# Optimization experiments

Hardware: AMD Instinct MI355X
Metric: run time of the kernel (lower is better)

## Reference

```python
import jax, jax.numpy as jnp
import numpy as np

N_NODES = 100000
N_EDGES = 1600000
D = 64

def setup_inputs() -> dict:
    key = jax.random.key(0)
    k1, k2, k3, k4 = jax.random.split(key, 4)
    feat = jax.random.normal(k1, (N_NODES, D), dtype=jnp.float32)
    src = jax.random.randint(k2, (N_EDGES,), 0, N_NODES, dtype=jnp.int32)
    dst = jax.random.randint(k3, (N_EDGES,), 0, N_NODES, dtype=jnp.int32)
    eps = jnp.zeros((1,), dtype=jnp.float32)
    W = jax.random.normal(k4, (D, D), dtype=jnp.float32) * (1.0 / np.sqrt(D))
    b = jnp.zeros((D,), dtype=jnp.float32)
    return {"feat": feat, "src": src, "dst": dst, "eps": eps, "W": W, "b": b}

def reference(feat, src, dst, eps, W, b):
    # GIN: h_i = f_Theta((1+eps)*h_i + sum_{j in N(i)} h_j)
    # Neighbor gather + segment-sum aggregation over edges (sum aggregator).
    msgs = feat[src]  # [E, D] gather of source node features
    agg = jax.ops.segment_sum(msgs, dst, num_segments=N_NODES)  # [N, D]
    rst = (1.0 + eps[0]) * feat + agg  # (1+eps)*self + aggregate
    # apply_func: Linear(D, D)
    return rst @ W + b
```

## Files before the change

### kernel.cpp

```cpp
#include <hip/hip_runtime.h>

#define NN 100000
#define NE 1600000
#define DD 64

#define NPB 128
#define NBUCK ((NN + NPB - 1) / NPB)
#define CAP 3072
#define OVF_CAP 4096
#define CHUNK 4096
#define NPART ((NE + CHUNK - 1) / CHUNK)


__global__ void __launch_bounds__(256) init_ws_kernel(int* __restrict__ gcur,
                                                      int* __restrict__ ovf_cnt) {
  int i = blockIdx.x * 256 + threadIdx.x;
  if (i < NBUCK) gcur[i] = i * CAP;
  if (i == 0) ovf_cnt[0] = 0;
}

__global__ void __launch_bounds__(256) partition_kernel(
    const int* __restrict__ src, const int* __restrict__ dst,
    int* __restrict__ gcur, int* __restrict__ ovf_cnt, int* __restrict__ ovf,
    unsigned int* __restrict__ sorted) {
  __shared__ int hist[NBUCK];
  __shared__ int base[NBUCK];
  int tid = threadIdx.x;
  int chunk = blockIdx.x * CHUNK;

  for (int i = tid; i < NBUCK; i += 256) hist[i] = 0;
  __syncthreads();

#pragma unroll
  for (int i = 0; i < CHUNK / 256; ++i) {
    int e = chunk + i * 256 + tid;
    if (e < NE) atomicAdd(&hist[dst[e] >> 7], 1);
  }
  __syncthreads();

  for (int i = tid; i < NBUCK; i += 256)
    base[i] = atomicAdd(&gcur[i], hist[i]);
  __syncthreads();

#pragma unroll
  for (int i = 0; i < CHUNK / 256; ++i) {
    int e = chunk + i * 256 + tid;
    if (e < NE) {
      int s = src[e], d = dst[e];
      int bk = d >> 7;
      int pos = atomicAdd(&base[bk], 1);
      if (pos < (bk + 1) * CAP) {
        sorted[pos] = ((unsigned int)s << 7) | (unsigned int)(d & 127);
      } else {
        int oi = atomicAdd(ovf_cnt, 1);
        if (oi < OVF_CAP) { ovf[2 * oi] = s; ovf[2 * oi + 1] = d; }
      }
    }
  }
}

__global__ void __launch_bounds__(256) bucket_agg2_kernel(
    const float* __restrict__ feat, const float* __restrict__ eps,
    const int* __restrict__ gcur, const unsigned int* __restrict__ sorted,
    float* __restrict__ out) {
  __shared__ int lhist[NPB];
  __shared__ int loffs[NPB];
  __shared__ int lcur[NPB];
  __shared__ int srcs[CAP];
  int tid = threadIdx.x;
  int bk = blockIdx.x;
  int base = bk * CAP;
  int cnt = gcur[bk] - base;
  if (cnt > CAP) cnt = CAP;
  const float4* f4 = reinterpret_cast<const float4*>(feat);

  if (tid < NPB) lhist[tid] = 0;
  __syncthreads();

  for (int i = tid; i < cnt; i += 256)
    atomicAdd(&lhist[sorted[base + i] & 127], 1);
  __syncthreads();

  if (tid < NPB) loffs[tid] = lhist[tid];
  __syncthreads();
  for (int off = 1; off < NPB; off <<= 1) {
    int t = 0;
    if (tid < NPB && tid >= off) t = loffs[tid - off];
    __syncthreads();
    if (tid < NPB) loffs[tid] += t;
    __syncthreads();
  }
  if (tid < NPB) lcur[tid] = loffs[tid] - lhist[tid];
  __syncthreads();

  for (int i = tid; i < cnt; i += 256) {
    unsigned int rec = sorted[base + i];
    int pos = atomicAdd(&lcur[rec & 127], 1);
    srcs[pos] = (int)(rec >> 7);
  }
  __syncthreads();

  float ec = 1.0f + eps[0];
  int grp = tid >> 4, q = tid & 15;
  int node0 = bk * NPB;
  for (int ln = grp; ln < NPB; ln += 16) {
    int row = node0 + ln;
    if (row >= NN) break;
    int s = loffs[ln] - lhist[ln];
    int e2 = loffs[ln];
    float4 sf = f4[(size_t)row * 16 + q];
    float ax = ec * sf.x, ay = ec * sf.y, az = ec * sf.z, aw = ec * sf.w;
    int k = s;
    for (; k + 4 <= e2; k += 4) {
      int s0 = srcs[k + 0], s1 = srcs[k + 1], s2 = srcs[k + 2], s3 = srcs[k + 3];
      float4 v0 = f4[(size_t)s0 * 16 + q];
      float4 v1 = f4[(size_t)s1 * 16 + q];
      float4 v2 = f4[(size_t)s2 * 16 + q];
      float4 v3 = f4[(size_t)s3 * 16 + q];
      ax += (v0.x + v1.x) + (v2.x + v3.x);
      ay += (v0.y + v1.y) + (v2.y + v3.y);
      az += (v0.z + v1.z) + (v2.z + v3.z);
      aw += (v0.w + v1.w) + (v2.w + v3.w);
    }
    for (; k < e2; ++k) {
      int s4 = srcs[k];
      float4 v = f4[(size_t)s4 * 16 + q];
      ax += v.x; ay += v.y; az += v.z; aw += v.w;
    }
    reinterpret_cast<float4*>(out)[(size_t)row * 16 + q] =
        make_float4(ax, ay, az, aw);
  }
}

__global__ void __launch_bounds__(256) ovf_fix_kernel(
    const float* __restrict__ feat, const int* __restrict__ ovf_cnt,
    const int* __restrict__ ovf, float* __restrict__ out) {
  int n = ovf_cnt[0];
  if (n > OVF_CAP) n = OVF_CAP;
  int t = blockIdx.x * blockDim.x + threadIdx.x;
  for (int i = t; i < n * 16; i += gridDim.x * blockDim.x) {
    int idx = i >> 4, q = i & 15;
    int s = ovf[2 * idx], d = ovf[2 * idx + 1];
    float4 v = reinterpret_cast<const float4*>(feat)[(size_t)s * 16 + q];
    float* op = out + (size_t)d * DD + q * 4;
    unsafeAtomicAdd(op + 0, v.x); unsafeAtomicAdd(op + 1, v.y);
    unsafeAtomicAdd(op + 2, v.z); unsafeAtomicAdd(op + 3, v.w);
  }
}

__global__ void __launch_bounds__(256) row_gemm3_kernel(float* __restrict__ out,
                                                        const float* __restrict__ W,
                                                        const float* __restrict__ b) {
  int lane = threadIdx.x & 63;
  int wid  = threadIdx.x >> 6;
  int g = blockIdx.x * 4 + wid;
  if (g >= NN / 16) return;
  int row0 = g * 16;

  float w[64];
#pragma unroll
  for (int k = 0; k < 64; ++k) w[k] = W[k * DD + lane];
  float bv = b[lane];

#pragma unroll
  for (int batch = 0; batch < 2; ++batch) {
    int rbase = row0 + batch * 8;
    float rst[8], acc[8];
#pragma unroll
    for (int r = 0; r < 8; ++r) rst[r] = out[(size_t)(rbase + r) * DD + lane];
#pragma unroll
    for (int r = 0; r < 8; ++r) acc[r] = bv;
#pragma unroll
    for (int k = 0; k < 64; ++k) {
#pragma unroll
      for (int r = 0; r < 8; ++r) {
        float s = __uint_as_float(__builtin_amdgcn_readlane(__float_as_uint(rst[r]), k));
        acc[r] = fmaf(s, w[k], acc[r]);
      }
    }
#pragma unroll
    for (int r = 0; r < 8; ++r) out[(size_t)(rbase + r) * DD + lane] = acc[r];
  }
}


constexpr int NB_SCAN = (NN + 1023) / 1024;

__global__ void __launch_bounds__(256) zero_kernel(int* __restrict__ p, int n) {
  int i = blockIdx.x * blockDim.x + threadIdx.x;
  if (i < n) p[i] = 0;
}

__global__ void __launch_bounds__(256) hist_kernel(const int* __restrict__ dst,
                                                   int* __restrict__ count) {
  int e = blockIdx.x * blockDim.x + threadIdx.x;
  atomicAdd(&count[dst[e]], 1);
}

__global__ void __launch_bounds__(1024) scan1_kernel(const int* __restrict__ count,
                                                     int* __restrict__ offsets,
                                                     int* __restrict__ bsums) {
  __shared__ int tmp[1024];
  int tid = threadIdx.x;
  int gid = blockIdx.x * 1024 + tid;
  int v = (gid < NN) ? count[gid] : 0;
  tmp[tid] = v;
  __syncthreads();
  for (int off = 1; off < 1024; off <<= 1) {
    int t = (tid >= off) ? tmp[tid - off] : 0;
    __syncthreads();
    tmp[tid] += t;
    __syncthreads();
  }
  if (gid < NN) offsets[gid] = tmp[tid] - v;
  if (tid == 1023) bsums[blockIdx.x] = tmp[1023];
}

__global__ void __launch_bounds__(128) scan2_kernel(int* __restrict__ bsums) {
  __shared__ int tmp[128];
  int tid = threadIdx.x;
  int v = (tid < NB_SCAN) ? bsums[tid] : 0;
  tmp[tid] = v;
  __syncthreads();
  for (int off = 1; off < 128; off <<= 1) {
    int t = (tid >= off) ? tmp[tid - off] : 0;
    __syncthreads();
    tmp[tid] += t;
    __syncthreads();
  }
  if (tid < NB_SCAN) bsums[tid] = tmp[tid] - v;
}

__global__ void __launch_bounds__(256) scan3_kernel(int* __restrict__ offsets,
                                                    const int* __restrict__ bsums,
                                                    int* __restrict__ cursor) {
  int gid = blockIdx.x * blockDim.x + threadIdx.x;
  if (gid < NN) {
    int o = offsets[gid] + bsums[gid >> 10];
    offsets[gid] = o;
    cursor[gid] = o;
  } else if (gid == NN) {
    offsets[NN] = NE;
  }
}

__global__ void __launch_bounds__(256) place_kernel(const int* __restrict__ src,
                                                    const int* __restrict__ dst,
                                                    int* __restrict__ cursor,
                                                    int* __restrict__ sorted) {
  int e = blockIdx.x * blockDim.x + threadIdx.x;
  int p = atomicAdd(&cursor[dst[e]], 1);
  sorted[p] = src[e];
}

__global__ void __launch_bounds__(256) pull4_kernel(const float* __restrict__ feat,
                                                    const float* __restrict__ eps,
                                                    const int* __restrict__ offsets,
                                                    const int* __restrict__ sorted,
                                                    float* __restrict__ out) {
  int t = blockIdx.x * blockDim.x + threadIdx.x;
  int node = t >> 4;
  int q = t & 15;
  const float4* f4 = reinterpret_cast<const float4*>(feat);

  int start = offsets[node];
  int end   = offsets[node + 1];
  float e = 1.0f + eps[0];
  float4 self = f4[(size_t)node * 16 + q];
  float ax = e * self.x, ay = e * self.y, az = e * self.z, aw = e * self.w;

  int k = start;
  for (; k + 4 <= end; k += 4) {
    int s0 = sorted[k + 0], s1 = sorted[k + 1], s2 = sorted[k + 2], s3 = sorted[k + 3];
    float4 v0 = f4[(size_t)s0 * 16 + q];
    float4 v1 = f4[(size_t)s1 * 16 + q];
    float4 v2 = f4[(size_t)s2 * 16 + q];
    float4 v3 = f4[(size_t)s3 * 16 + q];
    ax += (v0.x + v1.x) + (v2.x + v3.x);
    ay += (v0.y + v1.y) + (v2.y + v3.y);
    az += (v0.z + v1.z) + (v2.z + v3.z);
    aw += (v0.w + v1.w) + (v2.w + v3.w);
  }
  for (; k < end; ++k) {
    int s = sorted[k];
    float4 v = f4[(size_t)s * 16 + q];
    ax += v.x; ay += v.y; az += v.z; aw += v.w;
  }

  reinterpret_cast<float4*>(out)[(size_t)node * 16 + q] = make_float4(ax, ay, az, aw);
}


__global__ void __launch_bounds__(256) init_out_kernel(const float* __restrict__ feat,
                                                       const float* __restrict__ eps,
                                                       float* __restrict__ out) {
  int i = blockIdx.x * blockDim.x + threadIdx.x;
  float e = 1.0f + eps[0];
  float4 f = reinterpret_cast<const float4*>(feat)[i];
  reinterpret_cast<float4*>(out)[i] = make_float4(e * f.x, e * f.y, e * f.z, e * f.w);
}

__global__ void __launch_bounds__(256) scatter_edges_kernel(const float* __restrict__ feat,
                                                            const int* __restrict__ src,
                                                            const int* __restrict__ dst,
                                                            float* __restrict__ out) {
  int t = blockIdx.x * blockDim.x + threadIdx.x;
  int e = t >> 4;
  int q = t & 15;
  int s = src[e];
  int d = dst[e];
  float4 v = reinterpret_cast<const float4*>(feat)[s * 16 + q];
  float* op = out + d * DD + q * 4;
  atomicAdd(op + 0, v.x);
  atomicAdd(op + 1, v.y);
  atomicAdd(op + 2, v.z);
  atomicAdd(op + 3, v.w);
}


extern "C" void kernel_launch(void* const* d_in, const int* in_sizes, int n_in,
                              void* d_out, int out_size, void* d_ws, size_t ws_size,
                              hipStream_t stream) {
  const float* feat = (const float*)d_in[0];
  const int* src    = (const int*)d_in[1];
  const int* dst    = (const int*)d_in[2];
  const float* eps  = (const float*)d_in[3];
  const float* W    = (const float*)d_in[4];
  const float* b    = (const float*)d_in[5];
  float* out        = (float*)d_out;

  const int gemm_grid = (NN / 16 + 3) / 4;

  const size_t needA = ((size_t)NBUCK + 2 + 2 * OVF_CAP + (size_t)NBUCK * CAP) * sizeof(int);
  const size_t needB = ((size_t)3 * NN + 136 + NE) * sizeof(int);

  if (ws_size >= needA) {
    int* wsI = (int*)d_ws;
    int* gcur    = wsI;
    int* ovf_cnt = wsI + NBUCK;
    int* ovf     = wsI + NBUCK + 2;
    unsigned int* sorted = (unsigned int*)(wsI + NBUCK + 2 + 2 * OVF_CAP);

    init_ws_kernel<<<(NBUCK + 256) / 256, 256, 0, stream>>>(gcur, ovf_cnt);
    partition_kernel<<<NPART, 256, 0, stream>>>(src, dst, gcur, ovf_cnt, ovf, sorted);
    bucket_agg2_kernel<<<NBUCK, 256, 0, stream>>>(feat, eps, gcur, sorted, out);
    ovf_fix_kernel<<<8, 256, 0, stream>>>(feat, ovf_cnt, ovf, out);
    row_gemm3_kernel<<<gemm_grid, 256, 0, stream>>>(out, W, b);
  } else if (ws_size >= needB) {
    int* wsI     = (int*)d_ws;
    int* count   = wsI;
    int* offsets = wsI + NN;
    int* cursor  = wsI + 2 * NN + 8;
    int* bsums   = wsI + 3 * NN + 8;
    int* sortedB = wsI + 3 * NN + 136;

    zero_kernel<<<(NN + 255) / 256, 256, 0, stream>>>(count, NN);
    hist_kernel<<<NE / 256, 256, 0, stream>>>(dst, count);
    scan1_kernel<<<NB_SCAN, 1024, 0, stream>>>(count, offsets, bsums);
    scan2_kernel<<<1, 128, 0, stream>>>(bsums);
    scan3_kernel<<<(NN + 1 + 255) / 256, 256, 0, stream>>>(offsets, bsums, cursor);
    place_kernel<<<NE / 256, 256, 0, stream>>>(src, dst, cursor, sortedB);
    pull4_kernel<<<(NN * 16) / 256, 256, 0, stream>>>(feat, eps, offsets, sortedB, out);
    row_gemm3_kernel<<<gemm_grid, 256, 0, stream>>>(out, W, b);
  } else {
    init_out_kernel<<<(NN * DD / 4) / 256, 256, 0, stream>>>(feat, eps, out);
    scatter_edges_kernel<<<(NE * 16) / 256, 256, 0, stream>>>(feat, src, dst, out);
    row_gemm3_kernel<<<gemm_grid, 256, 0, stream>>>(out, W, b);
  }
}
```

Baseline: 207.1 us.

## Fuse overflow fix and linear layer into bucket aggregation, vectorize partition loads

The bucket aggregation kernel now keeps each bucket's aggregated rows in shared memory, applies any overflow edges there with shared atomics, and then runs the 64x64 linear transform before writing the output once. This removes the separate overflow-fix and GEMM kernels along with the global round trip of the intermediate result. The partition kernel loads src/dst as int4 and skips global atomics for empty buckets. In exchange, shared memory per block grows by about 34 KB, which may lower occupancy, and every block scans the whole overflow list serially when it is non-empty.

```diff
diff --git a/kernel.cpp b/kernel.cpp
--- a/kernel.cpp
+++ b/kernel.cpp
@@ -10,6 +10,8 @@
 #define OVF_CAP 4096
 #define CHUNK 4096
 #define NPART ((NE + CHUNK - 1) / CHUNK)
+#define NE4 (NE / 4)
+#define RPAD 68
 
 
 __global__ void __launch_bounds__(256) init_ws_kernel(int* __restrict__ gcur,
@@ -19,54 +21,74 @@
   if (i == 0) ovf_cnt[0] = 0;
 }
 
-__global__ void __launch_bounds__(256) partition_kernel(
+__global__ void __launch_bounds__(256) partition2_kernel(
     const int* __restrict__ src, const int* __restrict__ dst,
     int* __restrict__ gcur, int* __restrict__ ovf_cnt, int* __restrict__ ovf,
     unsigned int* __restrict__ sorted) {
   __shared__ int hist[NBUCK];
   __shared__ int base[NBUCK];
   int tid = threadIdx.x;
-  int chunk = blockIdx.x * CHUNK;
+  const int4* s4 = reinterpret_cast<const int4*>(src);
+  const int4* d4 = reinterpret_cast<const int4*>(dst);
+
+  int4 sv[4], dv[4];
+  int gi0 = blockIdx.x * 1024 + tid;
+#pragma unroll
+  for (int j = 0; j < 4; ++j) {
+    int gi = gi0 + j * 256;
+    if (gi < NE4) { sv[j] = s4[gi]; dv[j] = d4[gi]; }
+    else { sv[j] = make_int4(0, 0, 0, 0); dv[j] = make_int4(-1, -1, -1, -1); }
+  }
 
   for (int i = tid; i < NBUCK; i += 256) hist[i] = 0;
   __syncthreads();
 
 #pragma unroll
-  for (int i = 0; i < CHUNK / 256; ++i) {
-    int e = chunk + i * 256 + tid;
-    if (e < NE) atomicAdd(&hist[dst[e] >> 7], 1);
+  for (int j = 0; j < 4; ++j) {
+    int dd[4] = {dv[j].x, dv[j].y, dv[j].z, dv[j].w};
+#pragma unroll
+    for (int c = 0; c < 4; ++c)
+      if (dd[c] >= 0) atomicAdd(&hist[dd[c] >> 7], 1);
   }
   __syncthreads();
 
   for (int i = tid; i < NBUCK; i += 256)
-    base[i] = atomicAdd(&gcur[i], hist[i]);
-  __syncthreads();
-
-#pragma unroll
-  for (int i = 0; i < CHUNK / 256; ++i) {
-    int e = chunk + i * 256 + tid;
-    if (e < NE) {
-      int s = src[e], d = dst[e];
-      int bk = d >> 7;
-      int pos = atomicAdd(&base[bk], 1);
-      if (pos < (bk + 1) * CAP) {
-        sorted[pos] = ((unsigned int)s << 7) | (unsigned int)(d & 127);
-      } else {
-        int oi = atomicAdd(ovf_cnt, 1);
-        if (oi < OVF_CAP) { ovf[2 * oi] = s; ovf[2 * oi + 1] = d; }
+    base[i] = hist[i] ? atomicAdd(&gcur[i], hist[i]) : 0;
+  __syncthreads();
+
+#pragma unroll
+  for (int j = 0; j < 4; ++j) {
+    int dd[4] = {dv[j].x, dv[j].y, dv[j].z, dv[j].w};
+    int ss[4] = {sv[j].x, sv[j].y, sv[j].z, sv[j].w};
+#pragma unroll
+    for (int c = 0; c < 4; ++c) {
+      int d = dd[c];
+      if (d >= 0) {
+        int s = ss[c];
+        int bk = d >> 7;
+        int pos = atomicAdd(&base[bk], 1);
+        if (pos < (bk + 1) * CAP) {
+          sorted[pos] = ((unsigned int)s << 7) | (unsigned int)(d & 127);
+        } else {
+          int oi = atomicAdd(ovf_cnt, 1);
+          if (oi < OVF_CAP) { ovf[2 * oi] = s; ovf[2 * oi + 1] = d; }
+        }
       }
     }
   }
 }
 
-__global__ void __launch_bounds__(256) bucket_agg2_kernel(
+__global__ void __launch_bounds__(256) bucket_agg4_kernel(
     const float* __restrict__ feat, const float* __restrict__ eps,
     const int* __restrict__ gcur, const unsigned int* __restrict__ sorted,
+    const int* __restrict__ ovf_cnt, const int* __restrict__ ovf,
+    const float* __restrict__ W, const float* __restrict__ bvec,
     float* __restrict__ out) {
   __shared__ int lhist[NPB];
   __shared__ int loffs[NPB];
   __shared__ int lcur[NPB];
   __shared__ int srcs[CAP];
+  __shared__ float rst[NPB * RPAD];
   int tid = threadIdx.x;
   int bk = blockIdx.x;
   int base = bk * CAP;
@@ -123,28 +145,56 @@
       aw += (v0.w + v1.w) + (v2.w + v3.w);
     }
     for (; k < e2; ++k) {
-      int s4 = srcs[k];
-      float4 v = f4[(size_t)s4 * 16 + q];
+      int s4i = srcs[k];
+      float4 v = f4[(size_t)s4i * 16 + q];
       ax += v.x; ay += v.y; az += v.z; aw += v.w;
     }
-    reinterpret_cast<float4*>(out)[(size_t)row * 16 + q] =
+    *reinterpret_cast<float4*>(&rst[ln * RPAD + q * 4]) =
         make_float4(ax, ay, az, aw);
   }
-}
-
-__global__ void __launch_bounds__(256) ovf_fix_kernel(
-    const float* __restrict__ feat, const int* __restrict__ ovf_cnt,
-    const int* __restrict__ ovf, float* __restrict__ out) {
-  int n = ovf_cnt[0];
-  if (n > OVF_CAP) n = OVF_CAP;
-  int t = blockIdx.x * blockDim.x + threadIdx.x;
-  for (int i = t; i < n * 16; i += gridDim.x * blockDim.x) {
-    int idx = i >> 4, q = i & 15;
-    int s = ovf[2 * idx], d = ovf[2 * idx + 1];
-    float4 v = reinterpret_cast<const float4*>(feat)[(size_t)s * 16 + q];
-    float* op = out + (size_t)d * DD + q * 4;
-    unsafeAtomicAdd(op + 0, v.x); unsafeAtomicAdd(op + 1, v.y);
-    unsafeAtomicAdd(op + 2, v.z); unsafeAtomicAdd(op + 3, v.w);
+  __syncthreads();
+
+  int novf = ovf_cnt[0];
+  if (novf > 0) {
+    if (novf > OVF_CAP) novf = OVF_CAP;
+    for (int i = 0; i < novf; ++i) {
+      int d = ovf[2 * i + 1];
+      if ((d >> 7) == bk && tid < DD) {
+        int s = ovf[2 * i];
+        atomicAdd(&rst[(d & 127) * RPAD + tid], feat[(size_t)s * DD + tid]);
+      }
+    }
+    __syncthreads();
+  }
+
+  int lane = tid & 63;
+  int wid = tid >> 6;
+  float w[DD];
+#pragma unroll
+  for (int k = 0; k < DD; ++k) w[k] = W[k * DD + lane];
+  float bv = bvec[lane];
+
+#pragma unroll
+  for (int batch = 0; batch < 4; ++batch) {
+    int rb = wid * 32 + batch * 8;
+    float rv[8], acc[8];
+#pragma unroll
+    for (int r = 0; r < 8; ++r) rv[r] = rst[(rb + r) * RPAD + lane];
+#pragma unroll
+    for (int r = 0; r < 8; ++r) acc[r] = bv;
+#pragma unroll
+    for (int k = 0; k < DD; ++k) {
+#pragma unroll
+      for (int r = 0; r < 8; ++r) {
+        float s = __uint_as_float(__builtin_amdgcn_readlane(__float_as_uint(rv[r]), k));
+        acc[r] = fmaf(s, w[k], acc[r]);
+      }
+    }
+#pragma unroll
+    for (int r = 0; r < 8; ++r) {
+      int row = node0 + rb + r;
+      if (row < NN) out[(size_t)row * DD + lane] = acc[r];
+    }
   }
 }
 
@@ -165,16 +215,16 @@
 #pragma unroll
   for (int batch = 0; batch < 2; ++batch) {
     int rbase = row0 + batch * 8;
-    float rst[8], acc[8];
-#pragma unroll
-    for (int r = 0; r < 8; ++r) rst[r] = out[(size_t)(rbase + r) * DD + lane];
+    float rstv[8], acc[8];
+#pragma unroll
+    for (int r = 0; r < 8; ++r) rstv[r] = out[(size_t)(rbase + r) * DD + lane];
 #pragma unroll
     for (int r = 0; r < 8; ++r) acc[r] = bv;
 #pragma unroll
     for (int k = 0; k < 64; ++k) {
 #pragma unroll
       for (int r = 0; r < 8; ++r) {
-        float s = __uint_as_float(__builtin_amdgcn_readlane(__float_as_uint(rst[r]), k));
+        float s = __uint_as_float(__builtin_amdgcn_readlane(__float_as_uint(rstv[r]), k));
         acc[r] = fmaf(s, w[k], acc[r]);
       }
     }
@@ -342,10 +392,9 @@
     unsigned int* sorted = (unsigned int*)(wsI + NBUCK + 2 + 2 * OVF_CAP);
 
     init_ws_kernel<<<(NBUCK + 256) / 256, 256, 0, stream>>>(gcur, ovf_cnt);
-    partition_kernel<<<NPART, 256, 0, stream>>>(src, dst, gcur, ovf_cnt, ovf, sorted);
-    bucket_agg2_kernel<<<NBUCK, 256, 0, stream>>>(feat, eps, gcur, sorted, out);
-    ovf_fix_kernel<<<8, 256, 0, stream>>>(feat, ovf_cnt, ovf, out);
-    row_gemm3_kernel<<<gemm_grid, 256, 0, stream>>>(out, W, b);
+    partition2_kernel<<<NPART, 256, 0, stream>>>(src, dst, gcur, ovf_cnt, ovf, sorted);
+    bucket_agg4_kernel<<<NBUCK, 256, 0, stream>>>(feat, eps, gcur, sorted,
+                                                  ovf_cnt, ovf, W, b, out);
   } else if (ws_size >= needB) {
     int* wsI     = (int*)d_ws;
     int* count   = wsI;
```

New measurement: 244.1 us. 1.18x slower.

## Fuse overflow fix into GEMM, memset workspace, halve partition chunk size

Applied to the files above, without the earlier changes.

Replaces the init kernel with hipMemsetAsync and makes bucket cursors relative counts. The partition chunk size is halved to give more blocks, and empty buckets skip their global atomic. The overflow-fix kernel is folded into a new GEMM kernel that handles 8 rows per wave. Each wave scans the overflow list and adds matching edges before the matmul, which saves a launch and the global float atomics. The cost is a serial overflow scan per wave whenever overflow happens, and twice as many global cursor atomics from the smaller chunks.

```diff
diff --git a/kernel.cpp b/kernel.cpp
--- a/kernel.cpp
+++ b/kernel.cpp
@@ -8,18 +8,11 @@
 #define NBUCK ((NN + NPB - 1) / NPB)
 #define CAP 3072
 #define OVF_CAP 4096
-#define CHUNK 4096
+#define CHUNK 2048
 #define NPART ((NE + CHUNK - 1) / CHUNK)
 
 
-__global__ void __launch_bounds__(256) init_ws_kernel(int* __restrict__ gcur,
-                                                      int* __restrict__ ovf_cnt) {
-  int i = blockIdx.x * 256 + threadIdx.x;
-  if (i < NBUCK) gcur[i] = i * CAP;
-  if (i == 0) ovf_cnt[0] = 0;
-}
-
-__global__ void __launch_bounds__(256) partition_kernel(
+__global__ void __launch_bounds__(256) partition3_kernel(
     const int* __restrict__ src, const int* __restrict__ dst,
     int* __restrict__ gcur, int* __restrict__ ovf_cnt, int* __restrict__ ovf,
     unsigned int* __restrict__ sorted) {
@@ -38,8 +31,10 @@
   }
   __syncthreads();
 
-  for (int i = tid; i < NBUCK; i += 256)
-    base[i] = atomicAdd(&gcur[i], hist[i]);
+  for (int i = tid; i < NBUCK; i += 256) {
+    int h = hist[i];
+    base[i] = h ? atomicAdd(&gcur[i], h) : 0;
+  }
   __syncthreads();
 
 #pragma unroll
@@ -48,9 +43,9 @@
     if (e < NE) {
       int s = src[e], d = dst[e];
       int bk = d >> 7;
-      int pos = atomicAdd(&base[bk], 1);
-      if (pos < (bk + 1) * CAP) {
-        sorted[pos] = ((unsigned int)s << 7) | (unsigned int)(d & 127);
+      int r = atomicAdd(&base[bk], 1);
+      if (r < CAP) {
+        sorted[bk * CAP + r] = ((unsigned int)s << 7) | (unsigned int)(d & 127);
       } else {
         int oi = atomicAdd(ovf_cnt, 1);
         if (oi < OVF_CAP) { ovf[2 * oi] = s; ovf[2 * oi + 1] = d; }
@@ -70,7 +65,7 @@
   int tid = threadIdx.x;
   int bk = blockIdx.x;
   int base = bk * CAP;
-  int cnt = gcur[bk] - base;
+  int cnt = gcur[bk];
   if (cnt > CAP) cnt = CAP;
   const float4* f4 = reinterpret_cast<const float4*>(feat);
 
@@ -123,8 +118,8 @@
       aw += (v0.w + v1.w) + (v2.w + v3.w);
     }
     for (; k < e2; ++k) {
-      int s4 = srcs[k];
-      float4 v = f4[(size_t)s4 * 16 + q];
+      int s4i = srcs[k];
+      float4 v = f4[(size_t)s4i * 16 + q];
       ax += v.x; ay += v.y; az += v.z; aw += v.w;
     }
     reinterpret_cast<float4*>(out)[(size_t)row * 16 + q] =
@@ -132,20 +127,46 @@
   }
 }
 
-__global__ void __launch_bounds__(256) ovf_fix_kernel(
-    const float* __restrict__ feat, const int* __restrict__ ovf_cnt,
-    const int* __restrict__ ovf, float* __restrict__ out) {
-  int n = ovf_cnt[0];
-  if (n > OVF_CAP) n = OVF_CAP;
-  int t = blockIdx.x * blockDim.x + threadIdx.x;
-  for (int i = t; i < n * 16; i += gridDim.x * blockDim.x) {
-    int idx = i >> 4, q = i & 15;
-    int s = ovf[2 * idx], d = ovf[2 * idx + 1];
-    float4 v = reinterpret_cast<const float4*>(feat)[(size_t)s * 16 + q];
-    float* op = out + (size_t)d * DD + q * 4;
-    unsafeAtomicAdd(op + 0, v.x); unsafeAtomicAdd(op + 1, v.y);
-    unsafeAtomicAdd(op + 2, v.z); unsafeAtomicAdd(op + 3, v.w);
-  }
+__global__ void __launch_bounds__(256) row_gemm4_kernel(
+    float* __restrict__ out, const float* __restrict__ W,
+    const float* __restrict__ b, const int* __restrict__ ovf_cnt,
+    const int* __restrict__ ovf, const float* __restrict__ feat) {
+  int lane = threadIdx.x & 63;
+  int wid  = threadIdx.x >> 6;
+  int g = blockIdx.x * 4 + wid;
+  int row0 = g * 8;
+
+  float w[64];
+#pragma unroll
+  for (int k = 0; k < 64; ++k) w[k] = W[k * DD + lane];
+  float bv = b[lane];
+
+  float rstv[8], acc[8];
+#pragma unroll
+  for (int r = 0; r < 8; ++r) rstv[r] = out[(size_t)(row0 + r) * DD + lane];
+
+  int novf = ovf_cnt[0];
+  if (novf > 0) {
+    if (novf > OVF_CAP) novf = OVF_CAP;
+    for (int i = 0; i < novf; ++i) {
+      int d = ovf[2 * i + 1];
+      int r = d - row0;
+      if (r >= 0 && r < 8) rstv[r] += feat[(size_t)ovf[2 * i] * DD + lane];
+    }
+  }
+
+#pragma unroll
+  for (int r = 0; r < 8; ++r) acc[r] = bv;
+#pragma unroll
+  for (int k = 0; k < 64; ++k) {
+#pragma unroll
+    for (int r = 0; r < 8; ++r) {
+      float s = __uint_as_float(__builtin_amdgcn_readlane(__float_as_uint(rstv[r]), k));
+      acc[r] = fmaf(s, w[k], acc[r]);
+    }
+  }
+#pragma unroll
+  for (int r = 0; r < 8; ++r) out[(size_t)(row0 + r) * DD + lane] = acc[r];
 }
 
 __global__ void __launch_bounds__(256) row_gemm3_kernel(float* __restrict__ out,
@@ -165,16 +186,16 @@
 #pragma unroll
   for (int batch = 0; batch < 2; ++batch) {
     int rbase = row0 + batch * 8;
-    float rst[8], acc[8];
-#pragma unroll
-    for (int r = 0; r < 8; ++r) rst[r] = out[(size_t)(rbase + r) * DD + lane];
+    float rstv[8], acc[8];
+#pragma unroll
+    for (int r = 0; r < 8; ++r) rstv[r] = out[(size_t)(rbase + r) * DD + lane];
 #pragma unroll
     for (int r = 0; r < 8; ++r) acc[r] = bv;
 #pragma unroll
     for (int k = 0; k < 64; ++k) {
 #pragma unroll
       for (int r = 0; r < 8; ++r) {
-        float s = __uint_as_float(__builtin_amdgcn_readlane(__float_as_uint(rst[r]), k));
+        float s = __uint_as_float(__builtin_amdgcn_readlane(__float_as_uint(rstv[r]), k));
         acc[r] = fmaf(s, w[k], acc[r]);
       }
     }
@@ -329,8 +350,6 @@
   const float* b    = (const float*)d_in[5];
   float* out        = (float*)d_out;
 
-  const int gemm_grid = (NN / 16 + 3) / 4;
-
   const size_t needA = ((size_t)NBUCK + 2 + 2 * OVF_CAP + (size_t)NBUCK * CAP) * sizeof(int);
   const size_t needB = ((size_t)3 * NN + 136 + NE) * sizeof(int);
 
@@ -341,11 +360,10 @@
     int* ovf     = wsI + NBUCK + 2;
     unsigned int* sorted = (unsigned int*)(wsI + NBUCK + 2 + 2 * OVF_CAP);
 
-    init_ws_kernel<<<(NBUCK + 256) / 256, 256, 0, stream>>>(gcur, ovf_cnt);
-    partition_kernel<<<NPART, 256, 0, stream>>>(src, dst, gcur, ovf_cnt, ovf, sorted);
+    hipMemsetAsync(gcur, 0, (NBUCK + 2) * sizeof(int), stream);
+    partition3_kernel<<<NPART, 256, 0, stream>>>(src, dst, gcur, ovf_cnt, ovf, sorted);
     bucket_agg2_kernel<<<NBUCK, 256, 0, stream>>>(feat, eps, gcur, sorted, out);
-    ovf_fix_kernel<<<8, 256, 0, stream>>>(feat, ovf_cnt, ovf, out);
-    row_gemm3_kernel<<<gemm_grid, 256, 0, stream>>>(out, W, b);
+    row_gemm4_kernel<<<NN / 8 / 4, 256, 0, stream>>>(out, W, b, ovf_cnt, ovf, feat);
   } else if (ws_size >= needB) {
     int* wsI     = (int*)d_ws;
     int* count   = wsI;
@@ -361,10 +379,10 @@
     scan3_kernel<<<(NN + 1 + 255) / 256, 256, 0, stream>>>(offsets, bsums, cursor);
     place_kernel<<<NE / 256, 256, 0, stream>>>(src, dst, cursor, sortedB);
     pull4_kernel<<<(NN * 16) / 256, 256, 0, stream>>>(feat, eps, offsets, sortedB, out);
-    row_gemm3_kernel<<<gemm_grid, 256, 0, stream>>>(out, W, b);
+    row_gemm3_kernel<<<(NN / 16 + 3) / 4, 256, 0, stream>>>(out, W, b);
   } else {
     init_out_kernel<<<(NN * DD / 4) / 256, 256, 0, stream>>>(feat, eps, out);
     scatter_edges_kernel<<<(NE * 16) / 256, 256, 0, stream>>>(feat, src, dst, out);
-    row_gemm3_kernel<<<gemm_grid, 256, 0, stream>>>(out, W, b);
-  }
-}
+    row_gemm3_kernel<<<(NN / 16 + 3) / 4, 256, 0, stream>>>(out, W, b);
+  }
+}
```

Measured after the change: 217.0 us. +4.8%, slower.
